# Optimization experiments

Measured on AMD Instinct MI355X. Metric: run time of the kernel, lower is better.

The kernel has to match this reference:

```python
import jax, jax.numpy as jnp
import numpy as np

TOP_K = 2  # matches init_kwargs top_k


def setup_inputs() -> dict:
    key = jax.random.key(0)
    ks = jax.random.split(key, 7)
    d_model, d_ff, E = 512, 2048, 8
    B, S = 2, 2048
    std = 0.02
    return {
        "x": jax.random.normal(ks[0], (B, S, d_model), dtype=jnp.float32),
        "Wr": jax.random.normal(ks[1], (E, d_model), dtype=jnp.float32) * std,
        "br": jnp.zeros((E,), dtype=jnp.float32),
        "W1": jax.random.normal(ks[2], (E, d_model, d_ff), dtype=jnp.float32) * (1.0 / np.sqrt(d_model)),
        "b1": jnp.zeros((E, d_ff), dtype=jnp.float32),
        "W2": jax.random.normal(ks[3], (E, d_ff, d_model), dtype=jnp.float32) * (1.0 / np.sqrt(d_ff)),
        "b2": jnp.zeros((E, d_model), dtype=jnp.float32),
    }


def _moe_forward(x, Wr, br, W1, b1, W2, b2):
    leading = x.shape[:-1]
    d = x.shape[-1]
    E = Wr.shape[0]
    xf = x.reshape(-1, d)                                   # [N, d]
    N = xf.shape[0]

    # --- token router (linear head) ---
    logits = xf @ Wr.T + br                                  # [N, E]
    routing = jax.nn.softmax(logits, axis=-1)                # [N, E]
    sel_w, sel_idx = jax.lax.top_k(routing, TOP_K)           # [N, K]
    sel_w = sel_w / jnp.sum(sel_w, axis=-1, keepdims=True)   # renormalize top-k

    # combine weights as dense [N, E] (zero for unselected experts)
    combine = jnp.zeros((N, E), dtype=xf.dtype).at[
        jnp.arange(N)[:, None], sel_idx
    ].add(sel_w)                                             # [N, E]

    # --- expert FFNs (dense all-expert compute, masked combine) ---
    h = jax.nn.gelu(jnp.einsum("nd,edf->enf", xf, W1) + b1[:, None, :])  # [E, N, ff]
    y = jnp.einsum("enf,efd->end", h, W2) + b2[:, None, :]               # [E, N, d]

    out = jnp.einsum("ne,end->nd", combine, y)               # [N, d]
    return out.reshape(*leading, d)


def reference(x, Wr, br, W1, b1, W2, b2):
    return _moe_forward(x, Wr, br, W1, b1, W2, b2)
```

## Files before the change

kernel.cpp:

```cpp
#include <hip/hip_runtime.h>
#include <hip/hip_bf16.h>
#include <cstdint>

typedef unsigned short u16;
typedef __bf16 bf16_t;
typedef __bf16 bf16x8 __attribute__((ext_vector_type(8)));
typedef float f32x4 __attribute__((ext_vector_type(4)));

#define DM   512
#define DFF  2048
#define NEXP 8

__device__ __forceinline__ u16 f2bf(float f) {
  bf16_t b = (bf16_t)f;
  return __builtin_bit_cast(u16, b);
}
__device__ __forceinline__ uint32_t pack_bf2(float lo, float hi) {
  return (uint32_t)f2bf(lo) | ((uint32_t)f2bf(hi) << 16);
}
__device__ __forceinline__ float gelu_tanh(float x) {
  float x3 = x * x * x;
  float z = 0.7978845608028654f * (x + 0.044715f * x3);
  float az = fabsf(z);
  float e = __expf(2.0f * az);
  float t = 1.0f - 2.0f / (e + 1.0f);
  t = copysignf(t, z);
  return 0.5f * x * (1.0f + t);
}
__device__ __forceinline__ void async16(const u16* g, u16* l) {
  __builtin_amdgcn_global_load_lds((const __attribute__((address_space(1))) void*)g,
                                   (__attribute__((address_space(3))) void*)l, 16, 0, 0);
}

__global__ void k_transpose_cvt(const float* __restrict__ src, u16* __restrict__ dst,
                                int R, int C) {
  __shared__ u16 tile[64][66];
  int e = blockIdx.y;
  int tilesC = C >> 6;
  int bR = (blockIdx.x / tilesC) << 6;
  int bC = (blockIdx.x % tilesC) << 6;
  const float* s = src + (size_t)e * R * C;
  u16* d = dst + (size_t)e * R * C;
  int rr = threadIdx.x >> 4;
  int cc = (threadIdx.x & 15) << 2;
#pragma unroll
  for (int i = 0; i < 4; ++i) {
    int r = (i << 4) + rr;
    float4 v = *(const float4*)(s + (size_t)(bR + r) * C + bC + cc);
    *(uint32_t*)&tile[r][cc]     = pack_bf2(v.x, v.y);
    *(uint32_t*)&tile[r][cc + 2] = pack_bf2(v.z, v.w);
  }
  __syncthreads();
  int c0 = threadIdx.x >> 5;
  int j  = (threadIdx.x & 31) << 1;
#pragma unroll
  for (int i = 0; i < 8; ++i) {
    int c = (i << 3) + c0;
    uint32_t v = (uint32_t)tile[j][c] | ((uint32_t)tile[j + 1][c] << 16);
    *(uint32_t*)(&d[(size_t)(bC + c) * R + bR + j]) = v;
  }
}

__global__ void k_router(const float* __restrict__ x, const float* __restrict__ Wr,
                         const float* __restrict__ br, int* __restrict__ sel_idx,
                         float* __restrict__ sel_w, int Ntok) {
  int wid = threadIdx.x >> 6;
  int lane = threadIdx.x & 63;
  int tok = (blockIdx.x << 2) + wid;
  if (tok >= Ntok) return;
  const float4* xr = (const float4*)(x + (size_t)tok * DM);
  float4 x0 = xr[lane * 2], x1 = xr[lane * 2 + 1];
  float logit[NEXP];
#pragma unroll
  for (int e = 0; e < NEXP; ++e) {
    const float4* wr = (const float4*)(Wr + e * DM);
    float4 w0 = wr[lane * 2], w1 = wr[lane * 2 + 1];
    float p = x0.x * w0.x + x0.y * w0.y + x0.z * w0.z + x0.w * w0.w
            + x1.x * w1.x + x1.y * w1.y + x1.z * w1.z + x1.w * w1.w;
#pragma unroll
    for (int off = 32; off; off >>= 1) p += __shfl_xor(p, off, 64);
    logit[e] = p + br[e];
  }
  if (lane == 0) {
    float mx = logit[0];
#pragma unroll
    for (int e = 1; e < NEXP; ++e) mx = fmaxf(mx, logit[e]);
    float pr[NEXP];
#pragma unroll
    for (int e = 0; e < NEXP; ++e) pr[e] = __expf(logit[e] - mx);
    int i0 = 0;
#pragma unroll
    for (int e = 1; e < NEXP; ++e) if (pr[e] > pr[i0]) i0 = e;
    int i1 = -1;
#pragma unroll
    for (int e = 0; e < NEXP; ++e) {
      if (e == i0) continue;
      if (i1 < 0 || pr[e] > pr[i1]) i1 = e;
    }
    float s2 = pr[i0] + pr[i1];
    sel_idx[tok * 2]     = i0;
    sel_idx[tok * 2 + 1] = i1;
    sel_w[tok * 2]       = pr[i0] / s2;
    sel_w[tok * 2 + 1]   = pr[i1] / s2;
  }
}

__global__ void k_scatter(const int* __restrict__ sel_idx, const float* __restrict__ sel_w,
                          int npairs, int* __restrict__ row_token, float* __restrict__ row_w,
                          int* __restrict__ pos_of, int* __restrict__ tileMeta,
                          int* __restrict__ gMeta) {
  __shared__ int cnt[NEXP], offs[NEXP], cur[NEXP];
  int tid = threadIdx.x;
  int lane = tid & 63;
  if (tid < NEXP) { cnt[tid] = 0; cur[tid] = 0; }
  __syncthreads();
  for (int p = tid; p < npairs; p += blockDim.x) {
    int e = sel_idx[p];
#pragma unroll
    for (int ex = 0; ex < NEXP; ++ex) {
      unsigned long long m = __ballot(e == ex);
      if (lane == 0 && m) atomicAdd(&cnt[ex], __popcll(m));
    }
  }
  __syncthreads();
  if (tid == 0) {
    int o = 0, nmt = 0;
    for (int e = 0; e < NEXP; ++e) {
      offs[e] = o;
      int c = cnt[e];
      int nt = (c + 127) >> 7;
      for (int t = 0; t < nt; ++t) {
        tileMeta[nmt * 3 + 0] = o + t * 128;
        tileMeta[nmt * 3 + 1] = o + c;
        tileMeta[nmt * 3 + 2] = e;
        ++nmt;
      }
      o += c;
    }
    gMeta[0] = nmt;
  }
  __syncthreads();
  for (int p = tid; p < npairs; p += blockDim.x) {
    int e = sel_idx[p];
    int pos = 0;
#pragma unroll
    for (int ex = 0; ex < NEXP; ++ex) {
      unsigned long long m = __ballot(e == ex);
      if (m) {
        int leader = __ffsll((long long)m) - 1;
        int base = 0;
        if (lane == leader) base = atomicAdd(&cur[ex], __popcll(m));
        base = __shfl(base, leader, 64);
        if (e == ex)
          pos = offs[ex] + base + __popcll(m & ((1ull << lane) - 1ull));
      }
    }
    row_token[pos] = p >> 1;
    row_w[pos] = sel_w[p];
    pos_of[p] = pos;
  }
}

__global__ void k_gather(const float* __restrict__ x, const int* __restrict__ row_token,
                         u16* __restrict__ Xg, int npairs) {
  int pos = (blockIdx.x << 2) + (threadIdx.x >> 6);
  int lane = threadIdx.x & 63;
  if (pos >= npairs) return;
  int tok = row_token[pos];
  const float4* src = (const float4*)(x + (size_t)tok * DM);
  float4 a = src[lane * 2], b = src[lane * 2 + 1];
  uint4 o;
  o.x = pack_bf2(a.x, a.y);
  o.y = pack_bf2(a.z, a.w);
  o.z = pack_bf2(b.x, b.y);
  o.w = pack_bf2(b.z, b.w);
  ((uint4*)(Xg + (size_t)pos * DM))[lane] = o;
}

template <int NFULL, int KTOT, int KCHUNK, bool GELU, bool SCALE, bool OUTBF16>
__launch_bounds__(256)
__global__ void k_gemm(const u16* __restrict__ A, const u16* __restrict__ BT,
                       const float* __restrict__ bias, const float* __restrict__ row_w,
                       void* __restrict__ Out, size_t pstride,
                       const int* __restrict__ tileMeta, const int* __restrict__ gMeta,
                       int maxmt) {
  constexpr int NT = NFULL / 128;
  constexpr int NK = KCHUNK / 32;
  int NB = gridDim.x;
  int bid = blockIdx.x;
  int wg = ((NB & 7) == 0) ? ((bid & 7) * (NB >> 3) + (bid >> 3)) : bid;
  int nt = wg % NT;
  int rem = wg / NT;
  int mt = rem % maxmt;
  int split = rem / maxmt;
  if (mt >= gMeta[0]) return;
  int posStart = tileMeta[mt * 3 + 0];
  int segEnd   = tileMeta[mt * 3 + 1];
  int e        = tileMeta[mt * 3 + 2];

  __shared__ __align__(16) u16 smem[24576];

  int tid = threadIdx.x, lane = tid & 63, wid = tid >> 6;
  int wm = wid >> 1, wn = wid & 1;

  const u16* Abase = A + (size_t)split * KCHUNK;
  const u16* Bbase = BT + ((size_t)e * NFULL + (size_t)nt * 128) * KTOT + (size_t)split * KCHUNK;

  int l4 = lane >> 2, c4 = lane & 3;
  const u16* aS[2];
  const u16* bS[2];
#pragma unroll
  for (int i = 0; i < 2; ++i) {
    int r = i * 64 + wid * 16 + l4;
    int gra = posStart + r;
    if (gra >= segEnd) gra = segEnd - 1;
    int cs = c4 ^ ((r >> 1) & 3);
    aS[i] = Abase + (size_t)gra * KTOT + cs * 8;
    bS[i] = Bbase + (size_t)r * KTOT + cs * 8;
  }

  auto stage = [&](int kt, int buf) {
    u16* as = smem + buf * 8192;
    u16* bs = as + 4096;
#pragma unroll
    for (int i = 0; i < 2; ++i) {
      async16(aS[i] + kt * 32, as + i * 2048 + wid * 512);
      async16(bS[i] + kt * 32, bs + i * 2048 + wid * 512);
    }
  };

  f32x4 acc[4][4] = {};

  stage(0, 0);
  stage(1, 1);
  int bufC = 0, bufS = 2;
#pragma unroll 1
  for (int t = 0; t < NK; ++t) {
    if (t + 1 < NK) asm volatile("s_waitcnt vmcnt(4)" ::: "memory");
    else            asm volatile("s_waitcnt vmcnt(0)" ::: "memory");
    __builtin_amdgcn_s_barrier();
    asm volatile("" ::: "memory");
    if (t + 2 < NK) { stage(t + 2, bufS); bufS = (bufS == 2) ? 0 : bufS + 1; }
    const char* AsB = (const char*)(smem + bufC * 8192);
    const char* BsB = AsB + 8192;
    int kb = (lane >> 4) << 4;
    bf16x8 av[4], bv[4];
#pragma unroll
    for (int mi = 0; mi < 4; ++mi) {
      int row = (wm << 6) + (mi << 4) + (lane & 15);
      av[mi] = *(const bf16x8*)(AsB + row * 64 + (kb ^ (((row >> 1) & 3) << 4)));
    }
#pragma unroll
    for (int ni = 0; ni < 4; ++ni) {
      int row = (wn << 6) + (ni << 4) + (lane & 15);
      bv[ni] = *(const bf16x8*)(BsB + row * 64 + (kb ^ (((row >> 1) & 3) << 4)));
    }
    __builtin_amdgcn_s_setprio(1);
#pragma unroll
    for (int mi = 0; mi < 4; ++mi)
#pragma unroll
      for (int ni = 0; ni < 4; ++ni)
        acc[mi][ni] = __builtin_amdgcn_mfma_f32_16x16x32_bf16(av[mi], bv[ni], acc[mi][ni], 0, 0, 0);
    __builtin_amdgcn_s_setprio(0);
    bufC = (bufC == 2) ? 0 : bufC + 1;
  }

  int laneCol = lane & 15;
  int laneRow4 = (lane >> 4) << 2;
  const float* biasE = bias + (size_t)e * NFULL;

  if constexpr (OUTBF16) {
    __syncthreads();
    u16* Cs = smem;
#pragma unroll
    for (int mi = 0; mi < 4; ++mi) {
#pragma unroll
      for (int j = 0; j < 4; ++j) {
        int r = (wm << 6) + (mi << 4) + laneRow4 + j;
#pragma unroll
        for (int ni = 0; ni < 4; ++ni) {
          int cl = (wn << 6) + (ni << 4) + laneCol;
          float v = acc[mi][ni][j] + biasE[(nt << 7) + cl];
          if constexpr (GELU) v = gelu_tanh(v);
          Cs[r * 136 + cl] = f2bf(v);
        }
      }
    }
    __syncthreads();
    int r0 = tid >> 4, q = tid & 15;
    u16* OutU = (u16*)Out;
#pragma unroll
    for (int i = 0; i < 8; ++i) {
      int r = (i << 4) + r0;
      if (posStart + r < segEnd)
        *((uint4*)(OutU + (size_t)(posStart + r) * NFULL + (nt << 7)) + q) =
            ((uint4*)(Cs + (size_t)r * 136))[q];
    }
  } else {
    float* OutF = (float*)Out + (size_t)split * pstride;
#pragma unroll
    for (int mi = 0; mi < 4; ++mi) {
#pragma unroll
      for (int j = 0; j < 4; ++j) {
        int m = posStart + (wm << 6) + (mi << 4) + laneRow4 + j;
        if (m < segEnd) {
          float w = 1.0f;
          if constexpr (SCALE) w = row_w[m];
#pragma unroll
          for (int ni = 0; ni < 4; ++ni) {
            int n = (nt << 7) + (wn << 6) + (ni << 4) + laneCol;
            float v = acc[mi][ni][j] + (split == 0 ? biasE[n] : 0.0f);
            OutF[(size_t)m * NFULL + n] = v * w;
          }
        }
      }
    }
  }
}

__global__ void k_combine(const float* __restrict__ P, size_t pstride,
                          const int* __restrict__ pos_of, float* __restrict__ out, int Ntok) {
  int tok = (blockIdx.x << 2) + (threadIdx.x >> 6);
  int lane = threadIdx.x & 63;
  if (tok >= Ntok) return;
  int p0 = pos_of[tok * 2], p1 = pos_of[tok * 2 + 1];
  const float4* a0 = (const float4*)(P + (size_t)p0 * DM);
  const float4* a1 = (const float4*)(P + pstride + (size_t)p0 * DM);
  const float4* b0 = (const float4*)(P + (size_t)p1 * DM);
  const float4* b1 = (const float4*)(P + pstride + (size_t)p1 * DM);
  float4* o = (float4*)(out + (size_t)tok * DM);
#pragma unroll
  for (int i = 0; i < 2; ++i) {
    int idx = lane * 2 + i;
    float4 x0 = a0[idx], x1 = a1[idx], y0 = b0[idx], y1 = b1[idx];
    o[idx] = make_float4(x0.x + x1.x + y0.x + y1.x,
                         x0.y + x1.y + y0.y + y1.y,
                         x0.z + x1.z + y0.z + y1.z,
                         x0.w + x1.w + y0.w + y1.w);
  }
}

extern "C" void kernel_launch(void* const* d_in, const int* in_sizes, int n_in,
                              void* d_out, int out_size, void* d_ws, size_t ws_size,
                              hipStream_t stream) {
  const float* x  = (const float*)d_in[0];
  const float* Wr = (const float*)d_in[1];
  const float* br = (const float*)d_in[2];
  const float* W1 = (const float*)d_in[3];
  const float* b1 = (const float*)d_in[4];
  const float* W2 = (const float*)d_in[5];
  const float* b2 = (const float*)d_in[6];
  float* out = (float*)d_out;

  int Ntok = in_sizes[0] / DM;
  int npairs = Ntok * 2;
  int maxmt = npairs / 128 + NEXP;
  size_t pstride = (size_t)npairs * DM;

  char* p = (char*)d_ws;
  u16* W1T = (u16*)p;  p += (size_t)NEXP * DFF * DM * 2;
  u16* W2T = (u16*)p;  p += (size_t)NEXP * DM * DFF * 2;
  u16* Xg  = (u16*)p;  p += (size_t)npairs * DM * 2;
  u16* H   = (u16*)p;  p += (size_t)npairs * DFF * 2;
  float* Part = (float*)p; p += 2 * pstride * 4;
  int* sel_idx   = (int*)p;   p += (size_t)npairs * 4;
  float* sel_w   = (float*)p; p += (size_t)npairs * 4;
  int* pos_of    = (int*)p;   p += (size_t)npairs * 4;
  int* row_token = (int*)p;   p += (size_t)npairs * 4;
  float* row_w   = (float*)p; p += (size_t)npairs * 4;
  int* tileMeta  = (int*)p;   p += (size_t)(maxmt * 3 + 16) * 4;
  int* gMeta     = (int*)p;   p += 64;

  k_transpose_cvt<<<dim3((DM / 64) * (DFF / 64), NEXP), 256, 0, stream>>>(W1, W1T, DM, DFF);
  k_transpose_cvt<<<dim3((DFF / 64) * (DM / 64), NEXP), 256, 0, stream>>>(W2, W2T, DFF, DM);
  k_router<<<dim3((Ntok + 3) / 4), 256, 0, stream>>>(x, Wr, br, sel_idx, sel_w, Ntok);
  k_scatter<<<dim3(1), 1024, 0, stream>>>(sel_idx, sel_w, npairs, row_token, row_w,
                                          pos_of, tileMeta, gMeta);
  k_gather<<<dim3(npairs / 4), 256, 0, stream>>>(x, row_token, Xg, npairs);
  k_gemm<DFF, DM, DM, true, false, true>
      <<<dim3(maxmt * (DFF / 128)), 256, 0, stream>>>(
          Xg, W1T, b1, nullptr, H, 0, tileMeta, gMeta, maxmt);
  k_gemm<DM, DFF, DFF / 2, false, true, false>
      <<<dim3(maxmt * (DM / 128) * 2), 256, 0, stream>>>(
          H, W2T, b2, row_w, Part, pstride, tileMeta, gMeta, maxmt);
  k_combine<<<dim3(Ntok / 4), 256, 0, stream>>>(Part, pstride, pos_of, out, Ntok);
}
```

Baseline: 144.4 us.

## Use 256-row expert tiles with 512-thread GEMMs and bf16 partial outputs

Replaces the 128x128 grouped GEMM with a templated 256-row tile kernel using 512 threads (8 waves) and a 64-wide K step with double buffering. Routing segments are now padded to 256-row tiles, and the second GEMM writes its split-K partials as bf16 through a swizzled LDS staging buffer, which halves partial-sum traffic into the combine kernel. Larger tiles improve operand reuse per block, but they waste more rows on small expert segments, reduce the number of blocks, and use more LDS and registers. Storing partials in bf16 also loses some precision.

```diff
diff --git a/kernel.cpp b/kernel.cpp
--- a/kernel.cpp
+++ b/kernel.cpp
@@ -128,9 +128,9 @@
     for (int e = 0; e < NEXP; ++e) {
       offs[e] = o;
       int c = cnt[e];
-      int nt = (c + 127) >> 7;
+      int nt = (c + 255) >> 8;
       for (int t = 0; t < nt; ++t) {
-        tileMeta[nmt * 3 + 0] = o + t * 128;
+        tileMeta[nmt * 3 + 0] = o + t * 256;
         tileMeta[nmt * 3 + 1] = o + c;
         tileMeta[nmt * 3 + 2] = e;
         ++nmt;
@@ -177,20 +177,32 @@
   ((uint4*)(Xg + (size_t)pos * DM))[lane] = o;
 }
 
-template <int NFULL, int KTOT, int KCHUNK, bool GELU, bool SCALE, bool OUTBF16>
-__launch_bounds__(256)
-__global__ void k_gemm(const u16* __restrict__ A, const u16* __restrict__ BT,
-                       const float* __restrict__ bias, const float* __restrict__ row_w,
-                       void* __restrict__ Out, size_t pstride,
-                       const int* __restrict__ tileMeta, const int* __restrict__ gMeta,
-                       int maxmt) {
-  constexpr int NT = NFULL / 128;
-  constexpr int NK = KCHUNK / 32;
+template <int BN, int WN, int NFULL, int KTOT, int NSPLIT, bool GELU, bool SCALE>
+__launch_bounds__(512)
+__global__ void k_gemm256(const u16* __restrict__ A, const u16* __restrict__ BT,
+                          const float* __restrict__ bias, const float* __restrict__ row_w,
+                          u16* __restrict__ Out, size_t pstride,
+                          const int* __restrict__ tileMeta, const int* __restrict__ gMeta,
+                          int maxmt) {
+  constexpr int BM = 256;
+  constexpr int WM = 8 / WN;
+  constexpr int MI = BM / (WM * 16);
+  constexpr int NI = BN / (WN * 16);
+  constexpr int NTN = NFULL / BN;
+  constexpr int KCH = KTOT / NSPLIT;
+  constexpr int NK = KCH / 64;
+  constexpr int BUFB = (BM + BN) * 128;
+  constexpr int LA = 4;
+  constexpr int LB = (BN * 128) / 8192;
+  constexpr int IPH = BN / 128;
+
+  __shared__ __align__(16) char smem[2 * BUFB];
+
   int NB = gridDim.x;
   int bid = blockIdx.x;
   int wg = ((NB & 7) == 0) ? ((bid & 7) * (NB >> 3) + (bid >> 3)) : bid;
-  int nt = wg % NT;
-  int rem = wg / NT;
+  int nt = wg % NTN;
+  int rem = wg / NTN;
   int mt = rem % maxmt;
   int split = rem / maxmt;
   if (mt >= gMeta[0]) return;
@@ -198,146 +210,143 @@
   int segEnd   = tileMeta[mt * 3 + 1];
   int e        = tileMeta[mt * 3 + 2];
 
-  __shared__ __align__(16) u16 smem[24576];
-
   int tid = threadIdx.x, lane = tid & 63, wid = tid >> 6;
-  int wm = wid >> 1, wn = wid & 1;
-
-  const u16* Abase = A + (size_t)split * KCHUNK;
-  const u16* Bbase = BT + ((size_t)e * NFULL + (size_t)nt * 128) * KTOT + (size_t)split * KCHUNK;
-
-  int l4 = lane >> 2, c4 = lane & 3;
-  const u16* aS[2];
-  const u16* bS[2];
-#pragma unroll
-  for (int i = 0; i < 2; ++i) {
-    int r = i * 64 + wid * 16 + l4;
-    int gra = posStart + r;
-    if (gra >= segEnd) gra = segEnd - 1;
-    int cs = c4 ^ ((r >> 1) & 3);
-    aS[i] = Abase + (size_t)gra * KTOT + cs * 8;
-    bS[i] = Bbase + (size_t)r * KTOT + cs * 8;
-  }
-
-  auto stage = [&](int kt, int buf) {
-    u16* as = smem + buf * 8192;
-    u16* bs = as + 4096;
-#pragma unroll
-    for (int i = 0; i < 2; ++i) {
-      async16(aS[i] + kt * 32, as + i * 2048 + wid * 512);
-      async16(bS[i] + kt * 32, bs + i * 2048 + wid * 512);
-    }
+  int wm = wid / WN, wn = wid % WN;
+
+  const u16* Ab = A + (size_t)split * KCH;
+  const u16* Bb = BT + ((size_t)e * NFULL + (size_t)nt * BN) * KTOT + (size_t)split * KCH;
+
+  int trow = tid >> 2, tc = tid & 3;
+  const u16* aP[LA];
+  const u16* bP[LB];
+#pragma unroll
+  for (int a = 0; a < LA; ++a) {
+    int ks = a >> 1, r = ((a & 1) << 7) + trow;
+    int g = posStart + r;
+    if (g >= segEnd) g = segEnd - 1;
+    aP[a] = Ab + (size_t)g * KTOT + ks * 32 + ((tc ^ (r & 3)) << 3);
+  }
+#pragma unroll
+  for (int b = 0; b < LB; ++b) {
+    int ks = b / IPH, r = (b % IPH) * 128 + trow;
+    bP[b] = Bb + (size_t)r * KTOT + ks * 32 + ((tc ^ (r & 3)) << 3);
+  }
+
+  auto stage = [&](int t, int buf) {
+    char* dst = smem + buf * BUFB;
+#pragma unroll
+    for (int a = 0; a < LA; ++a)
+      async16(aP[a] + t * 64, (u16*)(dst + a * 8192 + tid * 16));
+#pragma unroll
+    for (int b = 0; b < LB; ++b)
+      async16(bP[b] + t * 64, (u16*)(dst + 32768 + b * 8192 + tid * 16));
   };
 
-  f32x4 acc[4][4] = {};
+  f32x4 acc[MI][NI] = {};
 
   stage(0, 0);
   stage(1, 1);
-  int bufC = 0, bufS = 2;
 #pragma unroll 1
   for (int t = 0; t < NK; ++t) {
-    if (t + 1 < NK) asm volatile("s_waitcnt vmcnt(4)" ::: "memory");
-    else            asm volatile("s_waitcnt vmcnt(0)" ::: "memory");
+    if (t == NK - 1)            asm volatile("s_waitcnt vmcnt(0)" ::: "memory");
+    else if constexpr (BN == 256) asm volatile("s_waitcnt vmcnt(8)" ::: "memory");
+    else                        asm volatile("s_waitcnt vmcnt(6)" ::: "memory");
     __builtin_amdgcn_s_barrier();
-    asm volatile("" ::: "memory");
-    if (t + 2 < NK) { stage(t + 2, bufS); bufS = (bufS == 2) ? 0 : bufS + 1; }
-    const char* AsB = (const char*)(smem + bufC * 8192);
-    const char* BsB = AsB + 8192;
-    int kb = (lane >> 4) << 4;
-    bf16x8 av[4], bv[4];
-#pragma unroll
-    for (int mi = 0; mi < 4; ++mi) {
-      int row = (wm << 6) + (mi << 4) + (lane & 15);
-      av[mi] = *(const bf16x8*)(AsB + row * 64 + (kb ^ (((row >> 1) & 3) << 4)));
-    }
-#pragma unroll
-    for (int ni = 0; ni < 4; ++ni) {
-      int row = (wn << 6) + (ni << 4) + (lane & 15);
-      bv[ni] = *(const bf16x8*)(BsB + row * 64 + (kb ^ (((row >> 1) & 3) << 4)));
-    }
-    __builtin_amdgcn_s_setprio(1);
-#pragma unroll
-    for (int mi = 0; mi < 4; ++mi)
-#pragma unroll
-      for (int ni = 0; ni < 4; ++ni)
-        acc[mi][ni] = __builtin_amdgcn_mfma_f32_16x16x32_bf16(av[mi], bv[ni], acc[mi][ni], 0, 0, 0);
-    __builtin_amdgcn_s_setprio(0);
-    bufC = (bufC == 2) ? 0 : bufC + 1;
-  }
-
-  int laneCol = lane & 15;
-  int laneRow4 = (lane >> 4) << 2;
+    const char* base = smem + (t & 1) * BUFB;
+#pragma unroll
+    for (int ks = 0; ks < 2; ++ks) {
+      bf16x8 av[MI], bv[NI];
+#pragma unroll
+      for (int mi = 0; mi < MI; ++mi) {
+        int r = wm * (MI * 16) + mi * 16 + (lane & 15);
+        av[mi] = *(const bf16x8*)(base + ks * 16384 + r * 64 +
+                                  (((lane >> 4) << 4) ^ ((r & 3) << 4)));
+      }
+#pragma unroll
+      for (int ni = 0; ni < NI; ++ni) {
+        int c = wn * (NI * 16) + ni * 16 + (lane & 15);
+        bv[ni] = *(const bf16x8*)(base + 32768 + ks * (BN * 64) + c * 64 +
+                                  (((lane >> 4) << 4) ^ ((c & 3) << 4)));
+      }
+      __builtin_amdgcn_s_setprio(1);
+#pragma unroll
+      for (int mi = 0; mi < MI; ++mi)
+#pragma unroll
+        for (int ni = 0; ni < NI; ++ni)
+          acc[mi][ni] = __builtin_amdgcn_mfma_f32_16x16x32_bf16(av[mi], bv[ni], acc[mi][ni], 0, 0, 0);
+      __builtin_amdgcn_s_setprio(0);
+    }
+    __builtin_amdgcn_s_barrier();
+    if (t + 2 < NK) stage(t + 2, t & 1);
+  }
+
+  constexpr int CR  = 65536 / (BN * 2);
+  constexpr int NCH = BM / CR;
   const float* biasE = bias + (size_t)e * NFULL;
-
-  if constexpr (OUTBF16) {
-    __syncthreads();
-    u16* Cs = smem;
-#pragma unroll
-    for (int mi = 0; mi < 4; ++mi) {
-#pragma unroll
-      for (int j = 0; j < 4; ++j) {
-        int r = (wm << 6) + (mi << 4) + laneRow4 + j;
-#pragma unroll
-        for (int ni = 0; ni < 4; ++ni) {
-          int cl = (wn << 6) + (ni << 4) + laneCol;
-          float v = acc[mi][ni][j] + biasE[(nt << 7) + cl];
-          if constexpr (GELU) v = gelu_tanh(v);
-          Cs[r * 136 + cl] = f2bf(v);
-        }
-      }
-    }
-    __syncthreads();
-    int r0 = tid >> 4, q = tid & 15;
-    u16* OutU = (u16*)Out;
-#pragma unroll
-    for (int i = 0; i < 8; ++i) {
-      int r = (i << 4) + r0;
-      if (posStart + r < segEnd)
-        *((uint4*)(OutU + (size_t)(posStart + r) * NFULL + (nt << 7)) + q) =
-            ((uint4*)(Cs + (size_t)r * 136))[q];
-    }
-  } else {
-    float* OutF = (float*)Out + (size_t)split * pstride;
-#pragma unroll
-    for (int mi = 0; mi < 4; ++mi) {
-#pragma unroll
-      for (int j = 0; j < 4; ++j) {
-        int m = posStart + (wm << 6) + (mi << 4) + laneRow4 + j;
-        if (m < segEnd) {
+  u16* OutS = Out + (size_t)split * pstride;
+#pragma unroll
+  for (int ch = 0; ch < NCH; ++ch) {
+    if (ch) __syncthreads();
+    if ((wm * (MI * 16)) / CR == ch) {
+#pragma unroll
+      for (int mi = 0; mi < MI; ++mi) {
+#pragma unroll
+        for (int j = 0; j < 4; ++j) {
+          int r = wm * (MI * 16) + mi * 16 + ((lane >> 4) << 2) + j;
+          int rl = r - ch * CR;
+          int m = posStart + r;
+          int mc = m < segEnd ? m : segEnd - 1;
           float w = 1.0f;
-          if constexpr (SCALE) w = row_w[m];
-#pragma unroll
-          for (int ni = 0; ni < 4; ++ni) {
-            int n = (nt << 7) + (wn << 6) + (ni << 4) + laneCol;
-            float v = acc[mi][ni][j] + (split == 0 ? biasE[n] : 0.0f);
-            OutF[(size_t)m * NFULL + n] = v * w;
+          if constexpr (SCALE) w = row_w[mc];
+#pragma unroll
+          for (int ni = 0; ni < NI; ++ni) {
+            int c = wn * (NI * 16) + ni * 16 + (lane & 15);
+            float v = acc[mi][ni][j];
+            if (split == 0) v += biasE[nt * BN + c];
+            if constexpr (GELU) v = gelu_tanh(v);
+            if constexpr (SCALE) v *= w;
+            *(u16*)(smem + rl * (BN * 2) + ((c * 2) ^ ((rl & 7) << 4))) = f2bf(v);
           }
         }
       }
     }
-  }
-}
-
-__global__ void k_combine(const float* __restrict__ P, size_t pstride,
+    __syncthreads();
+    constexpr int TPR = (BN * 2) / 128;
+    int rl = tid / TPR, cs0 = (tid % TPR) * 128;
+    int m = posStart + ch * CR + rl;
+    if (m < segEnd) {
+      uint4* dst = (uint4*)(OutS + (size_t)m * NFULL + nt * BN + (cs0 >> 1));
+#pragma unroll
+      for (int i = 0; i < 8; ++i) {
+        int cb = cs0 + i * 16;
+        dst[i] = *(const uint4*)(smem + rl * (BN * 2) + (cb ^ ((rl & 7) << 4)));
+      }
+    }
+  }
+}
+
+__global__ void k_combine(const u16* __restrict__ P, size_t pstride,
                           const int* __restrict__ pos_of, float* __restrict__ out, int Ntok) {
   int tok = (blockIdx.x << 2) + (threadIdx.x >> 6);
   int lane = threadIdx.x & 63;
   if (tok >= Ntok) return;
   int p0 = pos_of[tok * 2], p1 = pos_of[tok * 2 + 1];
-  const float4* a0 = (const float4*)(P + (size_t)p0 * DM);
-  const float4* a1 = (const float4*)(P + pstride + (size_t)p0 * DM);
-  const float4* b0 = (const float4*)(P + (size_t)p1 * DM);
-  const float4* b1 = (const float4*)(P + pstride + (size_t)p1 * DM);
-  float4* o = (float4*)(out + (size_t)tok * DM);
-#pragma unroll
-  for (int i = 0; i < 2; ++i) {
-    int idx = lane * 2 + i;
-    float4 x0 = a0[idx], x1 = a1[idx], y0 = b0[idx], y1 = b1[idx];
-    o[idx] = make_float4(x0.x + x1.x + y0.x + y1.x,
-                         x0.y + x1.y + y0.y + y1.y,
-                         x0.z + x1.z + y0.z + y1.z,
-                         x0.w + x1.w + y0.w + y1.w);
-  }
+  bf16x8 a0 = ((const bf16x8*)(P + (size_t)p0 * DM))[lane];
+  bf16x8 a1 = ((const bf16x8*)(P + pstride + (size_t)p0 * DM))[lane];
+  bf16x8 b0 = ((const bf16x8*)(P + (size_t)p1 * DM))[lane];
+  bf16x8 b1 = ((const bf16x8*)(P + pstride + (size_t)p1 * DM))[lane];
+  float4 o0, o1;
+  o0.x = (float)a0[0] + (float)a1[0] + (float)b0[0] + (float)b1[0];
+  o0.y = (float)a0[1] + (float)a1[1] + (float)b0[1] + (float)b1[1];
+  o0.z = (float)a0[2] + (float)a1[2] + (float)b0[2] + (float)b1[2];
+  o0.w = (float)a0[3] + (float)a1[3] + (float)b0[3] + (float)b1[3];
+  o1.x = (float)a0[4] + (float)a1[4] + (float)b0[4] + (float)b1[4];
+  o1.y = (float)a0[5] + (float)a1[5] + (float)b0[5] + (float)b1[5];
+  o1.z = (float)a0[6] + (float)a1[6] + (float)b0[6] + (float)b1[6];
+  o1.w = (float)a0[7] + (float)a1[7] + (float)b0[7] + (float)b1[7];
+  float4* o = (float4*)(out + (size_t)tok * DM + lane * 8);
+  o[0] = o0;
+  o[1] = o1;
 }
 
 extern "C" void kernel_launch(void* const* d_in, const int* in_sizes, int n_in,
@@ -354,7 +363,7 @@
 
   int Ntok = in_sizes[0] / DM;
   int npairs = Ntok * 2;
-  int maxmt = npairs / 128 + NEXP;
+  int maxmt = npairs / 256 + NEXP;
   size_t pstride = (size_t)npairs * DM;
 
   char* p = (char*)d_ws;
@@ -362,7 +371,7 @@
   u16* W2T = (u16*)p;  p += (size_t)NEXP * DM * DFF * 2;
   u16* Xg  = (u16*)p;  p += (size_t)npairs * DM * 2;
   u16* H   = (u16*)p;  p += (size_t)npairs * DFF * 2;
-  float* Part = (float*)p; p += 2 * pstride * 4;
+  u16* Part = (u16*)p; p += 2 * pstride * 2;
   int* sel_idx   = (int*)p;   p += (size_t)npairs * 4;
   float* sel_w   = (float*)p; p += (size_t)npairs * 4;
   int* pos_of    = (int*)p;   p += (size_t)npairs * 4;
@@ -377,11 +386,11 @@
   k_scatter<<<dim3(1), 1024, 0, stream>>>(sel_idx, sel_w, npairs, row_token, row_w,
                                           pos_of, tileMeta, gMeta);
   k_gather<<<dim3(npairs / 4), 256, 0, stream>>>(x, row_token, Xg, npairs);
-  k_gemm<DFF, DM, DM, true, false, true>
-      <<<dim3(maxmt * (DFF / 128)), 256, 0, stream>>>(
+  k_gemm256<256, 4, DFF, DM, 1, true, false>
+      <<<dim3(maxmt * (DFF / 256)), 512, 0, stream>>>(
           Xg, W1T, b1, nullptr, H, 0, tileMeta, gMeta, maxmt);
-  k_gemm<DM, DFF, DFF / 2, false, true, false>
-      <<<dim3(maxmt * (DM / 128) * 2), 256, 0, stream>>>(
+  k_gemm256<128, 2, DM, DFF, 2, false, true>
+      <<<dim3(maxmt * (DM / 128) * 2), 512, 0, stream>>>(
           H, W2T, b2, row_w, Part, pstride, tileMeta, gMeta, maxmt);
   k_combine<<<dim3(Ntok / 4), 256, 0, stream>>>(Part, pstride, pos_of, out, Ntok);
 }
```

Result: slower. 250.6 us (+73.5%).

## Fuse weight transposes, x conversion and router into one prep kernel; gather rows in GEMM

Applied to the files above, without the earlier changes.

The two weight transpose-convert kernels and the router merge into a single prep launch, which also converts x to bf16 once per token. The separate gather kernel is removed, and the first GEMM instead looks up each A row through row_token when setting up its async load addresses. This cuts launch count and avoids writing a duplicated gathered activation buffer. In exchange, the bf16 conversion of x now runs before routing is known, and the first GEMM reads A rows scattered by token index rather than contiguous.

```diff
diff --git a/kernel.cpp b/kernel.cpp
--- a/kernel.cpp
+++ b/kernel.cpp
@@ -32,15 +32,13 @@
                                    (__attribute__((address_space(3))) void*)l, 16, 0, 0);
 }
 
-__global__ void k_transpose_cvt(const float* __restrict__ src, u16* __restrict__ dst,
-                                int R, int C) {
+__device__ __forceinline__ void transpose_tile(const float* __restrict__ s,
+                                               u16* __restrict__ d, int R, int C,
+                                               int tileIdx) {
   __shared__ u16 tile[64][66];
-  int e = blockIdx.y;
   int tilesC = C >> 6;
-  int bR = (blockIdx.x / tilesC) << 6;
-  int bC = (blockIdx.x % tilesC) << 6;
-  const float* s = src + (size_t)e * R * C;
-  u16* d = dst + (size_t)e * R * C;
+  int bR = (tileIdx / tilesC) << 6;
+  int bC = (tileIdx % tilesC) << 6;
   int rr = threadIdx.x >> 4;
   int cc = (threadIdx.x & 15) << 2;
 #pragma unroll
@@ -61,12 +59,38 @@
   }
 }
 
-__global__ void k_router(const float* __restrict__ x, const float* __restrict__ Wr,
-                         const float* __restrict__ br, int* __restrict__ sel_idx,
-                         float* __restrict__ sel_w, int Ntok) {
+__global__ void k_prep(const float* __restrict__ W1, u16* __restrict__ W1T,
+                       const float* __restrict__ W2, u16* __restrict__ W2T,
+                       const float* __restrict__ x, u16* __restrict__ Xb,
+                       const float* __restrict__ Wr, const float* __restrict__ br,
+                       int* __restrict__ sel_idx, float* __restrict__ sel_w, int Ntok) {
+  int b = blockIdx.x;
+  if (b < 2048) {
+    int e = b >> 8, t = b & 255;
+    transpose_tile(W1 + (size_t)e * DM * DFF, W1T + (size_t)e * DM * DFF, DM, DFF, t);
+    return;
+  }
+  if (b < 4096) {
+    int e = (b - 2048) >> 8, t = (b - 2048) & 255;
+    transpose_tile(W2 + (size_t)e * DFF * DM, W2T + (size_t)e * DFF * DM, DFF, DM, t);
+    return;
+  }
+  if (b < 5120) {
+    size_t base = ((size_t)(b - 4096) << 11) + ((size_t)threadIdx.x << 3);
+    float4 a = *(const float4*)(x + base);
+    float4 c = *(const float4*)(x + base + 4);
+    uint4 o;
+    o.x = pack_bf2(a.x, a.y);
+    o.y = pack_bf2(a.z, a.w);
+    o.z = pack_bf2(c.x, c.y);
+    o.w = pack_bf2(c.z, c.w);
+    *(uint4*)(Xb + base) = o;
+    return;
+  }
+  int rb = b - 5120;
   int wid = threadIdx.x >> 6;
   int lane = threadIdx.x & 63;
-  int tok = (blockIdx.x << 2) + wid;
+  int tok = (rb << 2) + wid;
   if (tok >= Ntok) return;
   const float4* xr = (const float4*)(x + (size_t)tok * DM);
   float4 x0 = xr[lane * 2], x1 = xr[lane * 2 + 1];
@@ -161,25 +185,10 @@
   }
 }
 
-__global__ void k_gather(const float* __restrict__ x, const int* __restrict__ row_token,
-                         u16* __restrict__ Xg, int npairs) {
-  int pos = (blockIdx.x << 2) + (threadIdx.x >> 6);
-  int lane = threadIdx.x & 63;
-  if (pos >= npairs) return;
-  int tok = row_token[pos];
-  const float4* src = (const float4*)(x + (size_t)tok * DM);
-  float4 a = src[lane * 2], b = src[lane * 2 + 1];
-  uint4 o;
-  o.x = pack_bf2(a.x, a.y);
-  o.y = pack_bf2(a.z, a.w);
-  o.z = pack_bf2(b.x, b.y);
-  o.w = pack_bf2(b.z, b.w);
-  ((uint4*)(Xg + (size_t)pos * DM))[lane] = o;
-}
-
-template <int NFULL, int KTOT, int KCHUNK, bool GELU, bool SCALE, bool OUTBF16>
+template <int NFULL, int KTOT, int KCHUNK, bool GELU, bool SCALE, bool OUTBF16, bool USEMAP>
 __launch_bounds__(256)
-__global__ void k_gemm(const u16* __restrict__ A, const u16* __restrict__ BT,
+__global__ void k_gemm(const u16* __restrict__ A, const int* __restrict__ rowMap,
+                       const u16* __restrict__ BT,
                        const float* __restrict__ bias, const float* __restrict__ row_w,
                        void* __restrict__ Out, size_t pstride,
                        const int* __restrict__ tileMeta, const int* __restrict__ gMeta,
@@ -214,6 +223,7 @@
     int r = i * 64 + wid * 16 + l4;
     int gra = posStart + r;
     if (gra >= segEnd) gra = segEnd - 1;
+    if constexpr (USEMAP) gra = rowMap[gra];
     int cs = c4 ^ ((r >> 1) & 3);
     aS[i] = Abase + (size_t)gra * KTOT + cs * 8;
     bS[i] = Bbase + (size_t)r * KTOT + cs * 8;
@@ -360,7 +370,7 @@
   char* p = (char*)d_ws;
   u16* W1T = (u16*)p;  p += (size_t)NEXP * DFF * DM * 2;
   u16* W2T = (u16*)p;  p += (size_t)NEXP * DM * DFF * 2;
-  u16* Xg  = (u16*)p;  p += (size_t)npairs * DM * 2;
+  u16* Xb  = (u16*)p;  p += (size_t)Ntok * DM * 2;
   u16* H   = (u16*)p;  p += (size_t)npairs * DFF * 2;
   float* Part = (float*)p; p += 2 * pstride * 4;
   int* sel_idx   = (int*)p;   p += (size_t)npairs * 4;
@@ -371,17 +381,15 @@
   int* tileMeta  = (int*)p;   p += (size_t)(maxmt * 3 + 16) * 4;
   int* gMeta     = (int*)p;   p += 64;
 
-  k_transpose_cvt<<<dim3((DM / 64) * (DFF / 64), NEXP), 256, 0, stream>>>(W1, W1T, DM, DFF);
-  k_transpose_cvt<<<dim3((DFF / 64) * (DM / 64), NEXP), 256, 0, stream>>>(W2, W2T, DFF, DM);
-  k_router<<<dim3((Ntok + 3) / 4), 256, 0, stream>>>(x, Wr, br, sel_idx, sel_w, Ntok);
+  k_prep<<<dim3(5120 + Ntok / 4), 256, 0, stream>>>(W1, W1T, W2, W2T, x, Xb, Wr, br,
+                                                    sel_idx, sel_w, Ntok);
   k_scatter<<<dim3(1), 1024, 0, stream>>>(sel_idx, sel_w, npairs, row_token, row_w,
                                           pos_of, tileMeta, gMeta);
-  k_gather<<<dim3(npairs / 4), 256, 0, stream>>>(x, row_token, Xg, npairs);
-  k_gemm<DFF, DM, DM, true, false, true>
+  k_gemm<DFF, DM, DM, true, false, true, true>
       <<<dim3(maxmt * (DFF / 128)), 256, 0, stream>>>(
-          Xg, W1T, b1, nullptr, H, 0, tileMeta, gMeta, maxmt);
-  k_gemm<DM, DFF, DFF / 2, false, true, false>
+          Xb, row_token, W1T, b1, nullptr, H, 0, tileMeta, gMeta, maxmt);
+  k_gemm<DM, DFF, DFF / 2, false, true, false, false>
       <<<dim3(maxmt * (DM / 128) * 2), 256, 0, stream>>>(
-          H, W2T, b2, row_w, Part, pstride, tileMeta, gMeta, maxmt);
+          H, nullptr, W2T, b2, row_w, Part, pstride, tileMeta, gMeta, maxmt);
   k_combine<<<dim3(Ntok / 4), 256, 0, stream>>>(Part, pstride, pos_of, out, Ntok);
 }
```

Result: faster. 140.3 us (-2.9%).
